# Kernel optimization log

Measured on AMD Instinct MI355X. Metric: run time of the kernel, lower is better.

The kernel has to match this reference:

```python
import jax, jax.numpy as jnp
import numpy as np

IMG_W = 256; IMG_H = 256; N_PTS = 320
MIN_DEPTH = 3.0; MAX_DEPTH = 9.0; NDC_EXTENT = 1.0
SCALING = 0.1; EA_EPS = 1e-10; NORM_EPS = 1e-8


def setup_inputs() -> dict:
    key = jax.random.key(0)
    B, D = 1, 256
    image3d = jax.random.uniform(key, (B, 1, D, D, D), dtype=jnp.float32)
    # PyTorch3D convention: X_cam = X_world @ R + T. Camera at z=-6 world looking at origin.
    R = jnp.tile(jnp.eye(3, dtype=jnp.float32)[None], (B, 1, 1))
    T = jnp.tile(jnp.array([[0.0, 0.0, 6.0]], dtype=jnp.float32), (B, 1))
    focal = jnp.full((B,), 1.7320508, dtype=jnp.float32)  # NDC focal, fov ~ 60deg
    return {"image3d": image3d, "R": R, "T": T, "focal": focal}


def _trilinear_sample(vol, pts):
    # vol: [C, D, H, W]; pts: [N, 3] in xyz order, normalized coords in [-1, 1]
    # (grid_sample semantics: align_corners=True, padding_mode='zeros')
    C, D, H, W = vol.shape
    sizes = jnp.array([W, H, D], dtype=pts.dtype)
    idx = (pts + 1.0) * 0.5 * (sizes - 1.0)
    i0f = jnp.floor(idx)
    frac = idx - i0f
    i0 = i0f.astype(jnp.int32)
    volf = vol.reshape(C, -1)
    out = jnp.zeros((C, pts.shape[0]), dtype=vol.dtype)
    for dz in (0, 1):
        for dy in (0, 1):
            for dx in (0, 1):
                ix = i0[:, 0] + dx; iy = i0[:, 1] + dy; iz = i0[:, 2] + dz
                w = ((frac[:, 0] if dx else 1.0 - frac[:, 0]) *
                     (frac[:, 1] if dy else 1.0 - frac[:, 1]) *
                     (frac[:, 2] if dz else 1.0 - frac[:, 2]))
                valid = (ix >= 0) & (ix < W) & (iy >= 0) & (iy < H) & (iz >= 0) & (iz < D)
                lin = (jnp.clip(iz, 0, D - 1) * H + jnp.clip(iy, 0, H - 1)) * W + jnp.clip(ix, 0, W - 1)
                out = out + jnp.where(valid, w, 0.0)[None, :] * volf[:, lin]
    return out


def reference(image3d, R, T, focal):
    B, Cin, D, H, W = image3d.shape
    # features = image3d.repeat(1,3,1,1,1) when single channel
    features = jnp.broadcast_to(image3d, (B, 3, D, H, W)) if Cin == 1 else image3d
    densities = jnp.ones_like(image3d[:, :1]) * SCALING  # [B,1,D,H,W]
    shape = max(Cin, D)
    voxel_size = 2.0 * NDC_EXTENT / shape
    # Volumes local coords: world extent voxel_size*(size-1) maps to [-1,1]
    half_extent = jnp.array([voxel_size * (W - 1) / 2.0,
                             voxel_size * (H - 1) / 2.0,
                             voxel_size * (D - 1) / 2.0], dtype=image3d.dtype)
    # NDC pixel-center grid (PyTorch3D: +x left, +y up)
    xs = jnp.linspace(1.0 - 1.0 / IMG_W, -(1.0 - 1.0 / IMG_W), IMG_W, dtype=image3d.dtype)
    ys = jnp.linspace(1.0 - 1.0 / IMG_H, -(1.0 - 1.0 / IMG_H), IMG_H, dtype=image3d.dtype)
    depths = jnp.linspace(MIN_DEPTH, MAX_DEPTH, N_PTS, dtype=image3d.dtype)
    gy, gx = jnp.meshgrid(ys, xs, indexing="ij")  # [Hi, Wi]
    f = focal[:, None, None, None]
    dd = depths[None, None, None, :]
    x_cam = gx[None, :, :, None] * dd / f
    y_cam = gy[None, :, :, None] * dd / f
    z_cam = jnp.broadcast_to(dd, x_cam.shape)
    pts_cam = jnp.stack([x_cam, y_cam, z_cam], axis=-1)  # [B, Hi, Wi, P, 3]
    # unproject: X_world = (X_cam - T) @ R^T, i.e. X_world_i = sum_j (Xc - T)_j R_ij
    pts_world = jnp.einsum('bhwpj,bij->bhwpi', pts_cam - T[:, None, None, None, :], R)
    pts_local = pts_world / half_extent
    vol = jnp.concatenate([features, densities], axis=1)  # [B, 4, D, H, W]
    N = IMG_H * IMG_W * N_PTS
    vals = jax.vmap(_trilinear_sample)(vol, pts_local.reshape(B, N, 3))  # [B, 4, N]
    vals = vals.reshape(B, 4, IMG_H, IMG_W, N_PTS)
    feats = vals[:, :3]           # [B, 3, Hi, Wi, P]
    dens = vals[:, 3]             # [B, Hi, Wi, P]
    # EmissionAbsorption raymarcher: shifted cumprod absorption, alpha compositing
    cp = jnp.cumprod((1.0 + EA_EPS) - dens, axis=-1)
    absorption = jnp.concatenate([jnp.ones_like(cp[..., :1]), cp[..., :-1]], axis=-1)
    weights = dens * absorption
    rgb = jnp.einsum('bhwp,bchwp->bhwc', weights, feats)      # [B, Hi, Wi, 3]
    opacity = 1.0 - jnp.prod(1.0 - dens, axis=-1)             # [B, Hi, Wi]
    rgba = jnp.concatenate([rgb, opacity[..., None]], axis=-1)  # [B, Hi, Wi, 4]
    screen = jnp.transpose(rgba, (0, 3, 2, 1))                # [B, 4, Wi, Hi]
    gray = screen.mean(axis=1, keepdims=True)                 # is_grayscale=True
    return (gray + NORM_EPS) / (gray.max() + NORM_EPS)        # minimized()
```

## Files before the change

### kernel.cpp

```cpp
#include <hip/hip_runtime.h>

#define IMG_W 256
#define IMG_H 256
#define N_PTS 320
#define VD 256
#define VH 256
#define VW 256
#define DSTEP (6.0f / (N_PTS - 1))
#define TPX 16
#define CPR 16

__global__ __launch_bounds__(256) void render_kernel(
    const float* __restrict__ vol,
    const float* __restrict__ Rm, const float* __restrict__ Tv,
    const float* __restrict__ focal,
    float* __restrict__ out)
{
    const int tx = threadIdx.x;
    const int ty = threadIdx.y;
    const int w  = blockIdx.x * TPX + tx;
    const int h  = blockIdx.y;

    const float a  = 1.0f - 1.0f / IMG_W;
    const float gx = a - (2.0f * a / (IMG_W - 1)) * (float)w;
    const float gy = a - (2.0f * a / (IMG_H - 1)) * (float)h;
    const float f  = focal[0];
    const float ux = gx / f, uy = gy / f;
    const float R00 = Rm[0], R01 = Rm[1], R02 = Rm[2];
    const float R10 = Rm[3], R11 = Rm[4], R12 = Rm[5];
    const float R20 = Rm[6], R21 = Rm[7], R22 = Rm[8];
    const float Tx = Tv[0], Ty = Tv[1], Tz = Tv[2];
    const float Bx = R00 * ux + R01 * uy + R02;
    const float By = R10 * ux + R11 * uy + R12;
    const float Bz = R20 * ux + R21 * uy + R22;
    const float Ax = -(R00 * Tx + R01 * Ty + R02 * Tz);
    const float Ay = -(R10 * Tx + R11 * Ty + R12 * Tz);
    const float Az = -(R20 * Tx + R21 * Ty + R22 * Tz);
    const float voxel = 2.0f / 256.0f;
    const float hxe = voxel * (VW - 1) * 0.5f;
    const float hye = voxel * (VH - 1) * 0.5f;
    const float hze = voxel * (VD - 1) * 0.5f;
    const float sxc = 0.5f * (VW - 1) / hxe, oxc = 0.5f * (VW - 1);
    const float syc = 0.5f * (VH - 1) / hye, oyc = 0.5f * (VH - 1);
    const float szc = 0.5f * (VD - 1) / hze, ozc = 0.5f * (VD - 1);
    const float fBx = Bx * sxc, fAx = Ax * sxc + oxc;
    const float fBy = By * syc, fAy = Ay * syc + oyc;
    const float fBz = Bz * szc, fAz = Az * szc + ozc;

    float dlo = 3.0f, dhi = 9.0f;
    {
        const float lo = -1.0f, hi = 256.0f;
        const float fA[3] = { fAx, fAy, fAz };
        const float fB[3] = { fBx, fBy, fBz };
        #pragma unroll
        for (int dim = 0; dim < 3; ++dim) {
            if (fabsf(fB[dim]) > 1e-12f) {
                const float r = 1.0f / fB[dim];
                const float t0 = (lo - fA[dim]) * r, t1 = (hi - fA[dim]) * r;
                dlo = fmaxf(dlo, fminf(t0, t1));
                dhi = fminf(dhi, fmaxf(t0, t1));
            } else if (fA[dim] < lo || fA[dim] >= hi) {
                dhi = -1.0f;
            }
        }
    }
    int pmin = 0, len = 0;
    if (dhi > dlo) {
        pmin = max(0, (int)floorf((dlo - 3.0f) / DSTEP) - 1);
        const int pmax = min(N_PTS, (int)ceilf((dhi - 3.0f) / DSTEP) + 2);
        len = max(0, pmax - pmin);
    }

    const int plo = pmin + ((len * ty) >> 4);
    const int phi = pmin + ((len * (ty + 1)) >> 4);

    float S = 0.0f, A = 1.0f;
    for (int p = plo; p < phi; ++p) {
        const float d = 3.0f + (float)p * DSTEP;
        const float fx = fmaf(fBx, d, fAx);
        const float fy = fmaf(fBy, d, fAy);
        const float fz = fmaf(fBz, d, fAz);

        const float flx = floorf(fx), fly = floorf(fy), flz = floorf(fz);
        const int ix0 = (int)flx, iy0 = (int)fly, iz0 = (int)flz;

        float dens = 0.0f, feat = 0.0f;
        if (ix0 >= -1 && ix0 < VW && iy0 >= -1 && iy0 < VH && iz0 >= -1 && iz0 < VD) {
            const float frx = fx - flx, fry = fy - fly, frz = fz - flz;
            float wx0 = 1.0f - frx, wx1 = frx;
            float wy0 = 1.0f - fry, wy1 = fry;
            float wz0 = 1.0f - frz, wz1 = frz;
            if (ix0 < 0)       wx0 = 0.0f;
            if (ix0 + 1 >= VW) wx1 = 0.0f;
            if (iy0 < 0)       wy0 = 0.0f;
            if (iy0 + 1 >= VH) wy1 = 0.0f;
            if (iz0 < 0)       wz0 = 0.0f;
            if (iz0 + 1 >= VD) wz1 = 0.0f;

            const int cx0 = max(ix0, 0), cx1 = min(ix0 + 1, VW - 1);
            const int cy0 = max(iy0, 0), cy1 = min(iy0 + 1, VH - 1);
            const int cz0 = max(iz0, 0), cz1 = min(iz0 + 1, VD - 1);

            const int zb0 = cz0 * (VH * VW), zb1 = cz1 * (VH * VW);
            const int yb0 = cy0 * VW,        yb1 = cy1 * VW;

            const float v000 = vol[zb0 + yb0 + cx0];
            const float v001 = vol[zb0 + yb0 + cx1];
            const float v010 = vol[zb0 + yb1 + cx0];
            const float v011 = vol[zb0 + yb1 + cx1];
            const float v100 = vol[zb1 + yb0 + cx0];
            const float v101 = vol[zb1 + yb0 + cx1];
            const float v110 = vol[zb1 + yb1 + cx0];
            const float v111 = vol[zb1 + yb1 + cx1];

            const float w00 = wy0 * wz0, w01 = wy1 * wz0;
            const float w10 = wy0 * wz1, w11 = wy1 * wz1;
            const float c000 = wx0 * w00, c001 = wx1 * w00;
            const float c010 = wx0 * w01, c011 = wx1 * w01;
            const float c100 = wx0 * w10, c101 = wx1 * w10;
            const float c110 = wx0 * w11, c111 = wx1 * w11;

            feat = c000 * v000 + c001 * v001 + c010 * v010 + c011 * v011
                 + c100 * v100 + c101 * v101 + c110 * v110 + c111 * v111;
            dens = 0.1f * (c000 + c001 + c010 + c011 + c100 + c101 + c110 + c111);
        }

        S = fmaf(dens * A, feat, S);
        A *= (1.0f - dens);
    }

    __shared__ float lS[CPR][TPX];
    __shared__ float lA[CPR][TPX];
    lS[ty][tx] = S;
    lA[ty][tx] = A;
    __syncthreads();

    if (ty == 0) {
        float Stot = 0.0f, Atot = 1.0f;
        #pragma unroll
        for (int c = 0; c < CPR; ++c) {
            Stot = fmaf(Atot, lS[c][tx], Stot);
            Atot *= lA[c][tx];
        }
        const float gray = (3.0f * Stot + (1.0f - Atot)) * 0.25f;
        out[w * IMG_H + h] = gray;
    }
}

__global__ __launch_bounds__(1024) void maxnorm_kernel(float* __restrict__ out)
{
    float4* o4 = (float4*)out;
    const int tid = threadIdx.x;
    const int NV4 = (IMG_W * IMG_H) / 4;

    float4 v[16];
    float m = 0.0f;
    #pragma unroll
    for (int k = 0; k < 16; ++k) {
        v[k] = o4[tid + k * 1024];
        m = fmaxf(m, fmaxf(fmaxf(v[k].x, v[k].y), fmaxf(v[k].z, v[k].w)));
    }

    #pragma unroll
    for (int off = 32; off > 0; off >>= 1)
        m = fmaxf(m, __shfl_down(m, off));

    __shared__ float lm[16];
    if ((tid & 63) == 0) lm[tid >> 6] = m;
    __syncthreads();
    if (tid == 0) {
        float mm = lm[0];
        #pragma unroll
        for (int i = 1; i < 16; ++i) mm = fmaxf(mm, lm[i]);
        lm[0] = mm;
    }
    __syncthreads();
    const float inv = 1.0f / (lm[0] + 1e-8f);

    #pragma unroll
    for (int k = 0; k < 16; ++k) {
        float4 r;
        r.x = (v[k].x + 1e-8f) * inv;
        r.y = (v[k].y + 1e-8f) * inv;
        r.z = (v[k].z + 1e-8f) * inv;
        r.w = (v[k].w + 1e-8f) * inv;
        o4[tid + k * 1024] = r;
    }
    (void)NV4;
}

extern "C" void kernel_launch(void* const* d_in, const int* in_sizes, int n_in,
                              void* d_out, int out_size, void* d_ws, size_t ws_size,
                              hipStream_t stream) {
    (void)in_sizes; (void)n_in; (void)out_size; (void)d_ws; (void)ws_size;
    const float* vol   = (const float*)d_in[0];
    const float* Rm    = (const float*)d_in[1];
    const float* Tv    = (const float*)d_in[2];
    const float* focal = (const float*)d_in[3];
    float* out = (float*)d_out;

    dim3 rblock(TPX, CPR, 1);
    dim3 rgrid(IMG_W / TPX, IMG_H, 1);
    render_kernel<<<rgrid, rblock, 0, stream>>>(vol, Rm, Tv, focal, out);

    maxnorm_kernel<<<1, 1024, 0, stream>>>(out);
}
```

Measured before the change: 112.6 us.

## Compute per-block max in render kernel and parallelize normalization across blocks

The render kernel now does a shuffle reduction of the 16 gray values per block and writes one partial max per block to workspace. The single-block max/normalize kernel is replaced by a 64-block kernel where every block re-reduces the 4096 partial maxima and then normalizes its own float4 slice. This targets the serial single-workgroup tail that read and wrote the whole 64K-pixel image. The cost is redundant partial-max reads in each normalize block and a workspace buffer.

```diff
diff --git a/kernel.cpp b/kernel.cpp
--- a/kernel.cpp
+++ b/kernel.cpp
@@ -9,12 +9,15 @@
 #define DSTEP (6.0f / (N_PTS - 1))
 #define TPX 16
 #define CPR 16
+#define NBLK (IMG_W / TPX * IMG_H)
+
 
 __global__ __launch_bounds__(256) void render_kernel(
     const float* __restrict__ vol,
     const float* __restrict__ Rm, const float* __restrict__ Tv,
     const float* __restrict__ focal,
-    float* __restrict__ out)
+    float* __restrict__ out,
+    float* __restrict__ blkmax)
 {
     const int tx = threadIdx.x;
     const int ty = threadIdx.y;
@@ -144,64 +147,61 @@
         }
         const float gray = (3.0f * Stot + (1.0f - Atot)) * 0.25f;
         out[w * IMG_H + h] = gray;
+
+        float m = gray;
+        m = fmaxf(m, __shfl_down(m, 8));
+        m = fmaxf(m, __shfl_down(m, 4));
+        m = fmaxf(m, __shfl_down(m, 2));
+        m = fmaxf(m, __shfl_down(m, 1));
+        if (tx == 0)
+            blkmax[blockIdx.y * gridDim.x + blockIdx.x] = m;
     }
 }
 
-__global__ __launch_bounds__(1024) void maxnorm_kernel(float* __restrict__ out)
+__global__ __launch_bounds__(256) void normalize_kernel(
+    float* __restrict__ out, const float* __restrict__ blkmax)
 {
-    float4* o4 = (float4*)out;
     const int tid = threadIdx.x;
-    const int NV4 = (IMG_W * IMG_H) / 4;
-
-    float4 v[16];
+
     float m = 0.0f;
     #pragma unroll
-    for (int k = 0; k < 16; ++k) {
-        v[k] = o4[tid + k * 1024];
-        m = fmaxf(m, fmaxf(fmaxf(v[k].x, v[k].y), fmaxf(v[k].z, v[k].w)));
-    }
+    for (int k = 0; k < NBLK / 256; ++k)
+        m = fmaxf(m, blkmax[tid + k * 256]);
 
     #pragma unroll
     for (int off = 32; off > 0; off >>= 1)
         m = fmaxf(m, __shfl_down(m, off));
 
-    __shared__ float lm[16];
+    __shared__ float lm[4];
     if ((tid & 63) == 0) lm[tid >> 6] = m;
     __syncthreads();
-    if (tid == 0) {
-        float mm = lm[0];
-        #pragma unroll
-        for (int i = 1; i < 16; ++i) mm = fmaxf(mm, lm[i]);
-        lm[0] = mm;
-    }
-    __syncthreads();
-    const float inv = 1.0f / (lm[0] + 1e-8f);
-
-    #pragma unroll
-    for (int k = 0; k < 16; ++k) {
-        float4 r;
-        r.x = (v[k].x + 1e-8f) * inv;
-        r.y = (v[k].y + 1e-8f) * inv;
-        r.z = (v[k].z + 1e-8f) * inv;
-        r.w = (v[k].w + 1e-8f) * inv;
-        o4[tid + k * 1024] = r;
-    }
-    (void)NV4;
+    const float mm = fmaxf(fmaxf(lm[0], lm[1]), fmaxf(lm[2], lm[3]));
+    const float inv = 1.0f / (mm + 1e-8f);
+
+    float4* o4 = (float4*)out;
+    const int i = blockIdx.x * 256 + tid;
+    float4 v = o4[i];
+    v.x = (v.x + 1e-8f) * inv;
+    v.y = (v.y + 1e-8f) * inv;
+    v.z = (v.z + 1e-8f) * inv;
+    v.w = (v.w + 1e-8f) * inv;
+    o4[i] = v;
 }
 
 extern "C" void kernel_launch(void* const* d_in, const int* in_sizes, int n_in,
                               void* d_out, int out_size, void* d_ws, size_t ws_size,
                               hipStream_t stream) {
-    (void)in_sizes; (void)n_in; (void)out_size; (void)d_ws; (void)ws_size;
+    (void)in_sizes; (void)n_in; (void)out_size; (void)ws_size;
     const float* vol   = (const float*)d_in[0];
     const float* Rm    = (const float*)d_in[1];
     const float* Tv    = (const float*)d_in[2];
     const float* focal = (const float*)d_in[3];
     float* out = (float*)d_out;
+    float* blkmax = (float*)d_ws;
 
     dim3 rblock(TPX, CPR, 1);
     dim3 rgrid(IMG_W / TPX, IMG_H, 1);
-    render_kernel<<<rgrid, rblock, 0, stream>>>(vol, Rm, Tv, focal, out);
-
-    maxnorm_kernel<<<1, 1024, 0, stream>>>(out);
+    render_kernel<<<rgrid, rblock, 0, stream>>>(vol, Rm, Tv, focal, out, blkmax);
+
+    normalize_kernel<<<(IMG_W * IMG_H / 4) / 256, 256, 0, stream>>>(out, blkmax);
 }
```

Measured after the change: 109.0 us. 1.03x faster.
